# Optimization experiments

Hardware: AMD Instinct MI355X
Metric: run time of the kernel (lower is better)

The kernel has to match this reference:

```python
import jax, jax.numpy as jnp
import numpy as np

N_NODES, N_EDGES, D_IN, D_HID, D_OUT = 100000, 3200000, 128, 64, 10


def _gcn_norm(src, dst, n):
    # symmetric normalization deg^{-1/2}[src] * deg^{-1/2}[dst]; edge weights = 1
    ones = jnp.ones(src.shape[0], jnp.float32)
    deg = jax.ops.segment_sum(ones, dst, num_segments=n)
    dinv = jnp.where(deg > 0, jax.lax.rsqrt(jnp.maximum(deg, 1.0)), 0.0)
    return dinv[src] * dinv[dst]


def _gcn_conv(x, W, b, src, dst, norm, n):
    h = x @ W                                   # [N, out]
    msg = norm[:, None] * jnp.take(h, src, axis=0)  # [E+N, out]
    return jax.ops.segment_sum(msg, dst, num_segments=n) + b


def setup_inputs() -> dict:
    key = jax.random.key(0)
    ks = jax.random.split(key, 8)
    x = jax.random.normal(ks[0], (N_NODES, D_IN), jnp.float32)
    edge_index = jax.random.randint(ks[1], (2, N_EDGES), 0, N_NODES, jnp.int32)
    def glorot(k, fan_in, fan_out):
        s = (6.0 / (fan_in + fan_out)) ** 0.5
        return jax.random.uniform(k, (fan_in, fan_out), jnp.float32, -s, s)
    return {
        "x": x,
        "edge_index": edge_index,
        "W1": glorot(ks[2], D_IN, D_HID), "b1": jnp.zeros((D_HID,), jnp.float32),
        "W2": glorot(ks[3], D_HID, D_HID), "b2": jnp.zeros((D_HID,), jnp.float32),
        "W3": glorot(ks[4], D_HID, D_OUT), "b3": jnp.zeros((D_OUT,), jnp.float32),
    }


def reference(x, edge_index, W1, b1, W2, b2, W3, b3):
    n = x.shape[0]
    loops = jnp.arange(n, dtype=edge_index.dtype)
    src = jnp.concatenate([edge_index[0], loops])  # add self-loops (PyG default)
    dst = jnp.concatenate([edge_index[1], loops])
    norm = _gcn_norm(src, dst, n)                  # identical for all 3 layers
    h = jax.nn.relu(_gcn_conv(x, W1, b1, src, dst, norm, n))
    h = jax.nn.relu(_gcn_conv(h, W2, b2, src, dst, norm, n))
    return _gcn_conv(h, W3, b3, src, dst, norm, n)
```

## Files before the change

### kernel.cpp

```cpp
#include <hip/hip_runtime.h>


constexpr int BK_SHIFT = 6;
constexpr int BK_NODES = 64;
constexpr int BK_CAP   = 2432;
constexpr int MAXNB    = 1568;

typedef __attribute__((ext_vector_type(8))) short short8_t;
typedef __attribute__((ext_vector_type(4))) float f32x4_t;

__device__ __forceinline__ unsigned short f2bf(float f) {
    unsigned u = __builtin_bit_cast(unsigned, f);
    u += 0x7FFF + ((u >> 16) & 1);
    return (unsigned short)(u >> 16);
}
__device__ __forceinline__ unsigned pack2(float lo, float hi) {
    return (unsigned)f2bf(lo) | ((unsigned)f2bf(hi) << 16);
}
__device__ __forceinline__ float bf_lo(unsigned d) {
    return __builtin_bit_cast(float, d << 16);
}
__device__ __forceinline__ float bf_hi(unsigned d) {
    return __builtin_bit_cast(float, d & 0xFFFF0000u);
}
__device__ __forceinline__ float bf1(unsigned short u) {
    return __builtin_bit_cast(float, (unsigned)u << 16);
}

__global__ void k_partition(const int* __restrict__ src, const int* __restrict__ dst,
                            int E, int nb, int* __restrict__ cursor,
                            unsigned* __restrict__ inter) {
    __shared__ int lcount[MAXNB];
    __shared__ int gbase[MAXNB];
    int t = threadIdx.x;
    int base = blockIdx.x * 16384;
    for (int i = t; i < MAXNB; i += 512) lcount[i] = 0;
    __syncthreads();
    int sv[32], dvv[32];
#pragma unroll
    for (int j = 0; j < 32; j++) {
        int idx = base + j * 512 + t;
        if (idx < E) {
            sv[j] = src[idx]; dvv[j] = dst[idx];
            atomicAdd(&lcount[dvv[j] >> BK_SHIFT], 1);
        } else dvv[j] = -1;
    }
    __syncthreads();
    for (int i = t; i < nb; i += 512) {
        int c = lcount[i]; int g = 0;
        if (c) g = atomicAdd(&cursor[i], c);
        gbase[i] = g; lcount[i] = 0;
    }
    __syncthreads();
#pragma unroll
    for (int j = 0; j < 32; j++) {
        if (dvv[j] >= 0) {
            int b = dvv[j] >> BK_SHIFT;
            int r = gbase[b] + atomicAdd(&lcount[b], 1);
            if (r < BK_CAP)
                inter[(size_t)b * BK_CAP + r] =
                    (unsigned)sv[j] | ((unsigned)(dvv[j] & (BK_NODES - 1)) << 20);
        }
    }
}

__global__ __launch_bounds__(512) void k_sort(const unsigned* __restrict__ inter,
                        const int* __restrict__ cursor,
                        unsigned* __restrict__ srt_g, int* __restrict__ offs_g,
                        float* __restrict__ dinv, int N) {
    __shared__ unsigned raw[BK_CAP];
    __shared__ unsigned srt[BK_CAP];
    __shared__ int hist[BK_NODES];
    __shared__ int offs[BK_NODES + 1];
    __shared__ int cur[BK_NODES];
    int t = threadIdx.x, b = blockIdx.x;
    if (t < BK_NODES) hist[t] = 0;
    __syncthreads();
    int cnt = min(cursor[b], BK_CAP);
    const unsigned* ip = inter + (size_t)b * BK_CAP;
    for (int i = t; i < cnt; i += 512) {
        unsigned r = ip[i];
        raw[i] = r;
        atomicAdd(&hist[r >> 20], 1);
    }
    __syncthreads();
    if (t < BK_NODES) {
        int v = hist[t];
        int inc = v;
#pragma unroll
        for (int d = 1; d < 64; d <<= 1) {
            int o = __shfl_up(inc, d);
            if (t >= d) inc += o;
        }
        offs[t + 1] = inc;
        if (t == 0) offs[0] = 0;
        cur[t] = inc - v;
        int d = b * BK_NODES + t;
        if (d < N) dinv[d] = rsqrtf((float)(hist[t] + 1));
    }
    __syncthreads();
    for (int i = t; i < cnt; i += 512) {
        unsigned r = raw[i];
        int pos = atomicAdd(&cur[r >> 20], 1);
        srt[pos] = r & 0xFFFFFu;
    }
    __syncthreads();
    unsigned* sg = srt_g + (size_t)b * BK_CAP;
    for (int i = t; i < cnt; i += 512) sg[i] = srt[i];
    if (t < BK_NODES + 1) offs_g[b * (BK_NODES + 1) + t] = offs[t];
}

template <int K, bool IN_F32>
__global__ __launch_bounds__(256) void k_gemmMF(const void* __restrict__ Xv,
                           const float* __restrict__ W,
                           const float* __restrict__ dinv,
                           unsigned short* __restrict__ Y, int n) {
    constexpr int KP = K + 8;
    __shared__ unsigned short Al[64 * KP];
    __shared__ unsigned short Bl[64 * KP];
    int t = threadIdx.x;
    int nb = blockIdx.x * 64;
    if (IN_F32) {
        const float* X = (const float*)Xv;
        for (int i = t * 4; i < 64 * K; i += 1024) {
            int r = i / K, c = i % K;
            int node = nb + r;
            float4 v = {0.f, 0.f, 0.f, 0.f};
            if (node < n) v = *reinterpret_cast<const float4*>(X + (size_t)node * K + c);
            uint2 pk = {pack2(v.x, v.y), pack2(v.z, v.w)};
            *reinterpret_cast<uint2*>(&Al[r * KP + c]) = pk;
        }
    } else {
        const unsigned short* X = (const unsigned short*)Xv;
        for (int i = t * 4; i < 64 * K; i += 1024) {
            int r = i / K, c = i % K;
            int node = nb + r;
            uint2 pk = {0u, 0u};
            if (node < n) pk = *reinterpret_cast<const uint2*>(X + (size_t)node * K + c);
            *reinterpret_cast<uint2*>(&Al[r * KP + c]) = pk;
        }
    }
    {
        int c = t & 63, kb = t >> 6;
        for (int k = kb; k < K; k += 4)
            Bl[c * KP + k] = f2bf(W[k * 64 + c]);
    }
    __syncthreads();
    int w = t >> 6, lane = t & 63;
    int ml = lane & 15, kg = lane >> 4;
    f32x4_t acc[4] = {{0,0,0,0},{0,0,0,0},{0,0,0,0},{0,0,0,0}};
    for (int ks = 0; ks < K / 32; ks++) {
        int ko = ks * 32 + kg * 8;
        short8_t a = *reinterpret_cast<const short8_t*>(&Al[(16 * w + ml) * KP + ko]);
#pragma unroll
        for (int c = 0; c < 4; c++) {
            short8_t b = *reinterpret_cast<const short8_t*>(&Bl[(16 * c + ml) * KP + ko]);
            acc[c] = __builtin_amdgcn_mfma_f32_16x16x32_bf16(a, b, acc[c], 0, 0, 0);
        }
    }
#pragma unroll
    for (int r = 0; r < 4; r++) {
        int grow = nb + 16 * w + kg * 4 + r;
        if (grow < n) {
            float dv = dinv[grow];
#pragma unroll
            for (int c = 0; c < 4; c++)
                Y[((size_t)c * n + grow) * 16 + ml] = f2bf(dv * acc[c][r]);
        }
    }
}

__global__ void k_gemm10(const float* __restrict__ X, const float* __restrict__ W,
                         const float* __restrict__ dinv, unsigned short* __restrict__ Y, int n) {
    __shared__ float ws[64 * 10];
    __shared__ float xs[16 * 64];
    int t = threadIdx.x;
    for (int i = t; i < 640; i += 256) ws[i] = W[i];
    int nb = blockIdx.x * 16;
    for (int i = t; i < 16 * 64; i += 256) {
        int r = i >> 6, c = i & 63;
        int node = nb + r;
        xs[i] = (node < n) ? X[(size_t)node * 64 + c] : 0.f;
    }
    __syncthreads();
    int ns = t >> 4, c = t & 15;
    if (c < 10) {
        float acc = 0.f;
        for (int k = 0; k < 64; k++) acc += xs[ns * 64 + k] * ws[k * 10 + c];
        int node = nb + ns;
        if (node < n) Y[(size_t)node * 10 + c] = f2bf(dinv[node] * acc);
    }
}

template <int OBF>
__global__ __launch_bounds__(256) void k_agg64s(const unsigned short* __restrict__ Hs,
                        const unsigned* __restrict__ srt_g, const int* __restrict__ offs_g,
                        const float* __restrict__ dinv, const float* __restrict__ bias,
                        void* __restrict__ outv, int N, int nb, int relu) {
    __shared__ unsigned srt[BK_CAP];
    __shared__ int offs[BK_NODES + 1];
    int t = threadIdx.x;
    int x = blockIdx.x & 7;
    int q = x >> 1;
    int b = (blockIdx.x >> 3) * 2 + (x & 1);
    if (b >= nb) return;
    if (t < BK_NODES + 1) offs[t] = offs_g[b * (BK_NODES + 1) + t];
    __syncthreads();
    int cnt = offs[BK_NODES];
    const unsigned* sg = srt_g + (size_t)b * BK_CAP;
    for (int i = t; i < cnt; i += 256) srt[i] = sg[i];
    __syncthreads();
    const unsigned short* Hq = Hs + (size_t)q * N * 16;
    int wv = t >> 6, lane = t & 63;
    int nsub = lane >> 4;
    int slot = (lane >> 1) & 7;
    int cg   = lane & 1;
    const unsigned short* Hc = Hq + cg * 8;
    for (int g = wv * 4; g < BK_NODES; g += 16) {
        int nd = g + nsub;
        int d = b * BK_NODES + nd;
        bool valid = d < N;
        int o0 = valid ? offs[nd] : 0;
        int o1 = valid ? offs[nd + 1] : 0;
        float a0 = 0.f, a1 = 0.f, a2 = 0.f, a3 = 0.f;
        float a4 = 0.f, a5 = 0.f, a6 = 0.f, a7 = 0.f;
        int e = o0 + slot;
        for (; e + 8 < o1; e += 16) {
            int s0 = srt[e], s1 = srt[e + 8];
            const uint4 v0 = *reinterpret_cast<const uint4*>(Hc + (size_t)s0 * 16);
            const uint4 v1 = *reinterpret_cast<const uint4*>(Hc + (size_t)s1 * 16);
            a0 += bf_lo(v0.x); a1 += bf_hi(v0.x); a2 += bf_lo(v0.y); a3 += bf_hi(v0.y);
            a4 += bf_lo(v0.z); a5 += bf_hi(v0.z); a6 += bf_lo(v0.w); a7 += bf_hi(v0.w);
            a0 += bf_lo(v1.x); a1 += bf_hi(v1.x); a2 += bf_lo(v1.y); a3 += bf_hi(v1.y);
            a4 += bf_lo(v1.z); a5 += bf_hi(v1.z); a6 += bf_lo(v1.w); a7 += bf_hi(v1.w);
        }
        if (e < o1) {
            int s0 = srt[e];
            const uint4 v0 = *reinterpret_cast<const uint4*>(Hc + (size_t)s0 * 16);
            a0 += bf_lo(v0.x); a1 += bf_hi(v0.x); a2 += bf_lo(v0.y); a3 += bf_hi(v0.y);
            a4 += bf_lo(v0.z); a5 += bf_hi(v0.z); a6 += bf_lo(v0.w); a7 += bf_hi(v0.w);
        }
#pragma unroll
        for (int m = 2; m <= 8; m <<= 1) {
            a0 += __shfl_xor(a0, m); a1 += __shfl_xor(a1, m);
            a2 += __shfl_xor(a2, m); a3 += __shfl_xor(a3, m);
            a4 += __shfl_xor(a4, m); a5 += __shfl_xor(a5, m);
            a6 += __shfl_xor(a6, m); a7 += __shfl_xor(a7, m);
        }
        if (slot == 0 && valid) {
            float dv = dinv[d];
            const uint4 sv = *reinterpret_cast<const uint4*>(Hc + (size_t)d * 16);
            float s[8] = {bf_lo(sv.x), bf_hi(sv.x), bf_lo(sv.y), bf_hi(sv.y),
                          bf_lo(sv.z), bf_hi(sv.z), bf_lo(sv.w), bf_hi(sv.w)};
            float ac[8] = {a0, a1, a2, a3, a4, a5, a6, a7};
            const float* bp = bias + q * 16 + cg * 8;
            float o[8];
#pragma unroll
            for (int j = 0; j < 8; j++) {
                float val = dv * (ac[j] + s[j]) + bp[j];
                if (relu) val = fmaxf(val, 0.f);
                o[j] = val;
            }
            if (OBF) {
                unsigned short* op = (unsigned short*)outv + (size_t)d * 64 + q * 16 + cg * 8;
                uint4 pk = {pack2(o[0], o[1]), pack2(o[2], o[3]),
                            pack2(o[4], o[5]), pack2(o[6], o[7])};
                *reinterpret_cast<uint4*>(op) = pk;
            } else {
                float* op = (float*)outv + (size_t)d * 64 + q * 16 + cg * 8;
                float4 r0 = {o[0], o[1], o[2], o[3]}, r1 = {o[4], o[5], o[6], o[7]};
                *reinterpret_cast<float4*>(op)     = r0;
                *reinterpret_cast<float4*>(op + 4) = r1;
            }
        }
    }
}

__global__ __launch_bounds__(512) void k_agg10s(const unsigned short* __restrict__ H,
                        const unsigned* __restrict__ srt_g, const int* __restrict__ offs_g,
                        const float* __restrict__ dinv, const float* __restrict__ b3,
                        float* __restrict__ out, int N) {
    __shared__ unsigned srt[BK_CAP];
    __shared__ int offs[BK_NODES + 1];
    int t = threadIdx.x, b = blockIdx.x;
    if (t < BK_NODES + 1) offs[t] = offs_g[b * (BK_NODES + 1) + t];
    __syncthreads();
    int cnt = offs[BK_NODES];
    const unsigned* sg = srt_g + (size_t)b * BK_CAP;
    for (int i = t; i < cnt; i += 512) srt[i] = sg[i];
    __syncthreads();
    int wv = t >> 6, lane = t & 63;
    int es = lane >> 4, c = lane & 15;
    for (int nd = wv; nd < BK_NODES; nd += 8) {
        int d = b * BK_NODES + nd;
        if (d >= N) break;
        int o0 = offs[nd], o1 = offs[nd + 1];
        float acc = 0.f;
        if (c < 10) {
            int e = o0 + es;
            for (; e + 4 < o1; e += 8) {
                int s0 = srt[e], s1 = srt[e + 4];
                acc += bf1(H[(size_t)s0 * 10 + c]) + bf1(H[(size_t)s1 * 10 + c]);
            }
            if (e < o1) acc += bf1(H[(size_t)srt[e] * 10 + c]);
        }
        acc += __shfl_xor(acc, 16);
        acc += __shfl_xor(acc, 32);
        if (es == 0 && c < 10) {
            float dv = dinv[d];
            out[(size_t)d * 10 + c] = dv * (acc + bf1(H[(size_t)d * 10 + c])) + b3[c];
        }
    }
}

extern "C" void kernel_launch(void* const* d_in, const int* in_sizes, int n_in,
                              void* d_out, int out_size, void* d_ws, size_t ws_size,
                              hipStream_t stream) {
    const float* x  = (const float*)d_in[0];
    const int*   ei = (const int*)d_in[1];
    const float* W1 = (const float*)d_in[2];
    const float* b1 = (const float*)d_in[3];
    const float* W2 = (const float*)d_in[4];
    const float* b2 = (const float*)d_in[5];
    const float* W3 = (const float*)d_in[6];
    const float* b3 = (const float*)d_in[7];

    int N = in_sizes[0] / 128;
    int E = in_sizes[1] / 2;
    const int* esrc = ei;
    const int* edst = ei + E;
    int nb = (N + BK_NODES - 1) >> BK_SHIFT;

    char* p = (char*)d_ws;
    auto carve = [&](size_t bytes) -> void* {
        void* r = p;
        p += (bytes + 255) & ~(size_t)255;
        return r;
    };
    int*      cursor = (int*)carve((size_t)MAXNB * 4);
    unsigned* inter  = (unsigned*)carve((size_t)nb * BK_CAP * 4);
    unsigned* srt_g  = (unsigned*)carve((size_t)nb * BK_CAP * 4);
    int*      offs_g = (int*)carve((size_t)nb * (BK_NODES + 1) * 4);
    float*    dinv   = (float*)carve((size_t)N * 4);
    unsigned short* Hs = (unsigned short*)carve((size_t)N * 64 * 2);
    unsigned short* Gb = (unsigned short*)carve((size_t)N * 64 * 2);
    float*    Gf     = (float*)carve((size_t)N * 64 * 4);
    unsigned short* Hs10 = (unsigned short*)carve((size_t)N * 10 * 2);
    (void)ws_size; (void)n_in; (void)out_size;

    int gridA = ((nb + 1) / 2) * 8;

    hipMemsetAsync(cursor, 0, (size_t)nb * 4, stream);
    k_partition<<<(E + 16383) / 16384, 512, 0, stream>>>(esrc, edst, E, nb, cursor, inter);
    k_sort<<<nb, 512, 0, stream>>>(inter, cursor, srt_g, offs_g, dinv, N);

    k_gemmMF<128, true><<<(N + 63) / 64, 256, 0, stream>>>(x, W1, dinv, Hs, N);
    k_agg64s<1><<<gridA, 256, 0, stream>>>(Hs, srt_g, offs_g, dinv, b1, Gb, N, nb, 1);
    k_gemmMF<64, false><<<(N + 63) / 64, 256, 0, stream>>>(Gb, W2, dinv, Hs, N);
    k_agg64s<0><<<gridA, 256, 0, stream>>>(Hs, srt_g, offs_g, dinv, b2, Gf, N, nb, 1);
    k_gemm10<<<(N + 15) / 16, 256, 0, stream>>>(Gf, W3, dinv, Hs10, N);
    k_agg10s<<<nb, 512, 0, stream>>>(Hs10, srt_g, offs_g, dinv, b3, (float*)d_out, N);
}
```

Measured before the change: 270.6 us.

## Use row-major 64-wide hidden layout and one-block-per-bucket aggregation

The GEMM now writes hidden features row-major (node*64), not in four 16-column slabs. The 64-feature aggregation kernel changes to match: each 512-thread block handles a whole bucket, and each wave gathers full 128-byte rows with 8 lanes per edge covering all 64 columns. This removes the four-way re-read of each bucket's edge list and index staging, and makes each gathered row one contiguous 128-byte read. The cost is lower L2 locality than the slab layout, where each pass touched a 3.2 MB slice, and fewer blocks in the grid.

```diff
diff --git a/kernel.cpp b/kernel.cpp
--- a/kernel.cpp
+++ b/kernel.cpp
@@ -96,7 +96,7 @@
         if (t == 0) offs[0] = 0;
         cur[t] = inc - v;
         int d = b * BK_NODES + t;
-        if (d < N) dinv[d] = rsqrtf((float)(hist[t] + 1));
+        if (d < N) dinv[d] = rsqrtf((float)(v + 1));
     }
     __syncthreads();
     for (int i = t; i < cnt; i += 512) {
@@ -165,7 +165,7 @@
             float dv = dinv[grow];
 #pragma unroll
             for (int c = 0; c < 4; c++)
-                Y[((size_t)c * n + grow) * 16 + ml] = f2bf(dv * acc[c][r]);
+                Y[(size_t)grow * 64 + 16 * c + ml] = f2bf(dv * acc[c][r]);
         }
     }
 }
@@ -193,42 +193,39 @@
 }
 
 template <int OBF>
-__global__ __launch_bounds__(256) void k_agg64s(const unsigned short* __restrict__ Hs,
+__global__ __launch_bounds__(512) void k_agg64(const unsigned short* __restrict__ H,
                         const unsigned* __restrict__ srt_g, const int* __restrict__ offs_g,
                         const float* __restrict__ dinv, const float* __restrict__ bias,
-                        void* __restrict__ outv, int N, int nb, int relu) {
+                        void* __restrict__ outv, int N, int relu) {
     __shared__ unsigned srt[BK_CAP];
     __shared__ int offs[BK_NODES + 1];
-    int t = threadIdx.x;
-    int x = blockIdx.x & 7;
-    int q = x >> 1;
-    int b = (blockIdx.x >> 3) * 2 + (x & 1);
-    if (b >= nb) return;
+    int t = threadIdx.x, b = blockIdx.x;
     if (t < BK_NODES + 1) offs[t] = offs_g[b * (BK_NODES + 1) + t];
     __syncthreads();
     int cnt = offs[BK_NODES];
     const unsigned* sg = srt_g + (size_t)b * BK_CAP;
-    for (int i = t; i < cnt; i += 256) srt[i] = sg[i];
-    __syncthreads();
-    const unsigned short* Hq = Hs + (size_t)q * N * 16;
+    for (int i = t; i < cnt; i += 512) srt[i] = sg[i];
+    __syncthreads();
     int wv = t >> 6, lane = t & 63;
-    int nsub = lane >> 4;
-    int slot = (lane >> 1) & 7;
-    int cg   = lane & 1;
-    const unsigned short* Hc = Hq + cg * 8;
-    for (int g = wv * 4; g < BK_NODES; g += 16) {
-        int nd = g + nsub;
+    int esub = lane >> 3, cg = lane & 7;
+    const unsigned short* Hc = H + (cg << 3);
+    for (int nd = wv; nd < BK_NODES; nd += 8) {
         int d = b * BK_NODES + nd;
-        bool valid = d < N;
-        int o0 = valid ? offs[nd] : 0;
-        int o1 = valid ? offs[nd + 1] : 0;
+        if (d >= N) break;
+        int o0 = offs[nd], o1 = offs[nd + 1];
+        uint4 sv = {0, 0, 0, 0};
+        float dv = 0.f;
+        if (esub == 0) {
+            sv = *reinterpret_cast<const uint4*>(Hc + ((size_t)d << 6));
+            dv = dinv[d];
+        }
         float a0 = 0.f, a1 = 0.f, a2 = 0.f, a3 = 0.f;
         float a4 = 0.f, a5 = 0.f, a6 = 0.f, a7 = 0.f;
-        int e = o0 + slot;
+        int e = o0 + esub;
         for (; e + 8 < o1; e += 16) {
             int s0 = srt[e], s1 = srt[e + 8];
-            const uint4 v0 = *reinterpret_cast<const uint4*>(Hc + (size_t)s0 * 16);
-            const uint4 v1 = *reinterpret_cast<const uint4*>(Hc + (size_t)s1 * 16);
+            const uint4 v0 = *reinterpret_cast<const uint4*>(Hc + ((size_t)s0 << 6));
+            const uint4 v1 = *reinterpret_cast<const uint4*>(Hc + ((size_t)s1 << 6));
             a0 += bf_lo(v0.x); a1 += bf_hi(v0.x); a2 += bf_lo(v0.y); a3 += bf_hi(v0.y);
             a4 += bf_lo(v0.z); a5 += bf_hi(v0.z); a6 += bf_lo(v0.w); a7 += bf_hi(v0.w);
             a0 += bf_lo(v1.x); a1 += bf_hi(v1.x); a2 += bf_lo(v1.y); a3 += bf_hi(v1.y);
@@ -236,24 +233,22 @@
         }
         if (e < o1) {
             int s0 = srt[e];
-            const uint4 v0 = *reinterpret_cast<const uint4*>(Hc + (size_t)s0 * 16);
+            const uint4 v0 = *reinterpret_cast<const uint4*>(Hc + ((size_t)s0 << 6));
             a0 += bf_lo(v0.x); a1 += bf_hi(v0.x); a2 += bf_lo(v0.y); a3 += bf_hi(v0.y);
             a4 += bf_lo(v0.z); a5 += bf_hi(v0.z); a6 += bf_lo(v0.w); a7 += bf_hi(v0.w);
         }
 #pragma unroll
-        for (int m = 2; m <= 8; m <<= 1) {
+        for (int m = 8; m <= 32; m <<= 1) {
             a0 += __shfl_xor(a0, m); a1 += __shfl_xor(a1, m);
             a2 += __shfl_xor(a2, m); a3 += __shfl_xor(a3, m);
             a4 += __shfl_xor(a4, m); a5 += __shfl_xor(a5, m);
             a6 += __shfl_xor(a6, m); a7 += __shfl_xor(a7, m);
         }
-        if (slot == 0 && valid) {
-            float dv = dinv[d];
-            const uint4 sv = *reinterpret_cast<const uint4*>(Hc + (size_t)d * 16);
+        if (esub == 0) {
             float s[8] = {bf_lo(sv.x), bf_hi(sv.x), bf_lo(sv.y), bf_hi(sv.y),
                           bf_lo(sv.z), bf_hi(sv.z), bf_lo(sv.w), bf_hi(sv.w)};
             float ac[8] = {a0, a1, a2, a3, a4, a5, a6, a7};
-            const float* bp = bias + q * 16 + cg * 8;
+            const float* bp = bias + cg * 8;
             float o[8];
 #pragma unroll
             for (int j = 0; j < 8; j++) {
@@ -262,12 +257,12 @@
                 o[j] = val;
             }
             if (OBF) {
-                unsigned short* op = (unsigned short*)outv + (size_t)d * 64 + q * 16 + cg * 8;
+                unsigned short* op = (unsigned short*)outv + (size_t)d * 64 + cg * 8;
                 uint4 pk = {pack2(o[0], o[1]), pack2(o[2], o[3]),
                             pack2(o[4], o[5]), pack2(o[6], o[7])};
                 *reinterpret_cast<uint4*>(op) = pk;
             } else {
-                float* op = (float*)outv + (size_t)d * 64 + q * 16 + cg * 8;
+                float* op = (float*)outv + (size_t)d * 64 + cg * 8;
                 float4 r0 = {o[0], o[1], o[2], o[3]}, r1 = {o[4], o[5], o[6], o[7]};
                 *reinterpret_cast<float4*>(op)     = r0;
                 *reinterpret_cast<float4*>(op + 4) = r1;
@@ -348,16 +343,14 @@
     unsigned short* Hs10 = (unsigned short*)carve((size_t)N * 10 * 2);
     (void)ws_size; (void)n_in; (void)out_size;
 
-    int gridA = ((nb + 1) / 2) * 8;
-
     hipMemsetAsync(cursor, 0, (size_t)nb * 4, stream);
     k_partition<<<(E + 16383) / 16384, 512, 0, stream>>>(esrc, edst, E, nb, cursor, inter);
     k_sort<<<nb, 512, 0, stream>>>(inter, cursor, srt_g, offs_g, dinv, N);
 
     k_gemmMF<128, true><<<(N + 63) / 64, 256, 0, stream>>>(x, W1, dinv, Hs, N);
-    k_agg64s<1><<<gridA, 256, 0, stream>>>(Hs, srt_g, offs_g, dinv, b1, Gb, N, nb, 1);
+    k_agg64<1><<<nb, 512, 0, stream>>>(Hs, srt_g, offs_g, dinv, b1, Gb, N, 1);
     k_gemmMF<64, false><<<(N + 63) / 64, 256, 0, stream>>>(Gb, W2, dinv, Hs, N);
-    k_agg64s<0><<<gridA, 256, 0, stream>>>(Hs, srt_g, offs_g, dinv, b2, Gf, N, nb, 1);
+    k_agg64<0><<<nb, 512, 0, stream>>>(Hs, srt_g, offs_g, dinv, b2, Gf, N, 1);
     k_gemm10<<<(N + 15) / 16, 256, 0, stream>>>(Gf, W3, dinv, Hs10, N);
     k_agg10s<<<nb, 512, 0, stream>>>(Hs10, srt_g, offs_g, dinv, b3, (float*)d_out, N);
 }
```

Measured after the change: 245.4 us. 9.3% less time.
